# Kernel tuning notes

Measured on AMD Instinct MI355X. Metric: run time of the kernel, lower is better.

The kernel has to match this reference:

```python
import jax, jax.numpy as jnp
import numpy as np

K = 24          # num_eigh
D_MODEL = 768   # d_in == d_out
STATE = 100     # LDS state_dim
BSZ = 1
SEQ = 2048


def setup_inputs() -> dict:
    key = jax.random.key(0)
    ks = jax.random.split(key, 8)
    x = jax.random.normal(ks[0], (BSZ, SEQ, D_MODEL), dtype=jnp.float32)
    input_pos = jnp.arange(SEQ, dtype=jnp.int32)
    M_inputs = jax.random.normal(ks[1], (D_MODEL, D_MODEL), dtype=jnp.float32) * 0.02
    M_filters = jax.random.normal(ks[2], (K, D_MODEL), dtype=jnp.float32) * 0.02
    # LDS params: diagonal A (stable, |a|<1), B maps scalar input -> state,
    # C maps state -> 2K outputs, Dv is scalar-input feedthrough to 2K outputs.
    A = jax.random.uniform(ks[3], (STATE,), dtype=jnp.float32, minval=0.0, maxval=0.99)
    Bm = jax.random.normal(ks[4], (STATE,), dtype=jnp.float32) * 0.1
    C = jax.random.normal(ks[5], (STATE, 2 * K), dtype=jnp.float32) * 0.1
    Dv = jax.random.normal(ks[6], (2 * K,), dtype=jnp.float32) * 0.1
    return {"x": x, "input_pos": input_pos, "M_inputs": M_inputs,
            "M_filters": M_filters, "A": A, "Bm": Bm, "C": C, "Dv": Dv}


def reference(x, input_pos, M_inputs, M_filters, A, Bm, C, Dv):
    bsz, seq_len, d_in = x.shape
    k = M_filters.shape[0]
    # input projection (use_approx branch)
    xp = x @ M_inputs                                   # (b, s, d)
    # flatten per-channel scalar sequences: (b*d, s)
    u = xp.transpose(0, 2, 1).reshape(bsz * d_in, seq_len)
    ut = u.T                                            # (s, N) for scan over time
    h0 = jnp.zeros((bsz * d_in, A.shape[0]), dtype=xp.dtype)

    def step(h, u_t):
        # h: (N, state), u_t: (N,) scalar input per lane
        h = h * A[None, :] + u_t[:, None] * Bm[None, :]
        y = h @ C + u_t[:, None] * Dv[None, :]          # (N, 2K)
        return h, y

    _, ys = jax.lax.scan(step, h0, ut)                  # (s, N, 2K)
    # U: (b, s, 2K, d)
    U = ys.transpose(1, 0, 2).reshape(bsz, d_in, seq_len, 2 * k).transpose(0, 2, 3, 1)
    spectral_plus = jnp.einsum('bskd,kd->bsd', U[:, :, k:, :], M_filters)
    spectral_minus = jnp.einsum('bskd,kd->bsd', U[:, :, :k, :], M_filters)
    return spectral_plus + spectral_minus
```

## Files before the change

kernel.cpp:

```cpp
#include <hip/hip_runtime.h>

#define SEQ   2048
#define DM    768
#define ST    100
#define KF    24
#define NC    32
#define KJ    128
#define NJ    112
#define GK2   1536

using short8  = __attribute__((ext_vector_type(8))) short;
using float4v = __attribute__((ext_vector_type(4))) float;

__device__ __forceinline__ unsigned short bf16_rn(float x) {
    unsigned int u = __float_as_uint(x);
    unsigned int r = u + 0x7FFFu + ((u >> 16) & 1u);
    return (unsigned short)(r >> 16);
}
__device__ __forceinline__ float bf2f(unsigned short h) {
    return __uint_as_float(((unsigned int)h) << 16);
}
__device__ __forceinline__ void async16(const void* g, void* l) {
    __builtin_amdgcn_global_load_lds(
        (const __attribute__((address_space(1))) unsigned int*)g,
        (__attribute__((address_space(3))) unsigned int*)l, 16, 0, 0);
}

__global__ __launch_bounds__(256) void prep(const float* __restrict__ x,
                                            const float* __restrict__ Mi,
                                            const float* __restrict__ C,
                                            const float* __restrict__ Dv,
                                            const float* __restrict__ Mf,
                                            const float* __restrict__ Av,
                                            const float* __restrict__ Bv,
                                            unsigned short* __restrict__ Mbig,
                                            unsigned short* __restrict__ Xbig,
                                            float* __restrict__ WpT,
                                            float* __restrict__ evec,
                                            float* __restrict__ Apow,
                                            unsigned short* __restrict__ Ehi,
                                            unsigned short* __restrict__ Elo,
                                            unsigned short* __restrict__ Qhi,
                                            unsigned short* __restrict__ Qlo) {
    __shared__ float tl[64][65];
    int bid = blockIdx.x, t = threadIdx.x;
    if (bid < 144) {
        int i0 = (bid / 12) * 64, d0 = (bid % 12) * 64;
        int tx = t & 63, ty = t >> 6;
#pragma unroll
        for (int r = ty; r < 64; r += 4)
            tl[r][tx] = Mi[(i0 + r) * DM + d0 + tx];
        __syncthreads();
#pragma unroll
        for (int r = ty; r < 64; r += 4) {
            float v = tl[tx][r];
            unsigned short h = bf16_rn(v);
            unsigned short lo = bf16_rn(v - bf2f(h));
            unsigned short* row = Mbig + (size_t)(d0 + r) * GK2 + i0 + tx;
            row[0] = h; row[DM] = lo;
        }
    } else if (bid < 912) {
        int idx8 = (bid - 144) * 256 + t;
        int s = idx8 / (DM / 8), i0 = (idx8 % (DM / 8)) * 8;
        const float* xp = x + (size_t)s * DM + i0;
        float4 v0 = *(const float4*)xp;
        float4 v1 = *(const float4*)(xp + 4);
        float av[8] = {v0.x, v0.y, v0.z, v0.w, v1.x, v1.y, v1.z, v1.w};
        short8 hh;
#pragma unroll
        for (int q = 0; q < 8; ++q) hh[q] = (short)bf16_rn(av[q]);
        *(short8*)(Xbig + (size_t)s * DM + i0) = hh;
    } else if (bid < 1212) {
        int tid = (bid - 912) * 256 + t;
        if (tid < ST * DM) {
            int d = tid / ST, j = tid % ST;
            float s = 0.f;
#pragma unroll
            for (int k = 0; k < KF; ++k)
                s += (C[j * 2 * KF + k] + C[j * 2 * KF + KF + k]) * Mf[k * DM + d];
            WpT[tid] = s;
        }
        if (tid < DM) {
            float s = 0.f;
#pragma unroll
            for (int k = 0; k < KF; ++k)
                s += (Dv[k] + Dv[KF + k]) * Mf[k * DM + tid];
            evec[tid] = s;
        }
    } else {
        if (t < KJ) {
            bool ja = (t < ST);
            float a = ja ? Av[t] : 0.f;
            float b = ja ? Bv[t] : 0.f;
            float p = 1.f;
            for (int dlt = 0; dlt < 64; ++dlt) {
                if (ja) Apow[dlt * ST + t] = p;
                if (t < NJ) {
                    float v = b * p;
                    unsigned short h = bf16_rn(v);
                    Qhi[t * 64 + 63 - dlt] = h;
                    Qlo[t * 64 + 63 - dlt] = bf16_rn(v - bf2f(h));
                }
                p *= a;
                unsigned short h = bf16_rn(p);
                Ehi[dlt * KJ + t] = h;
                Elo[dlt * KJ + t] = bf16_rn(p - bf2f(h));
            }
            if (ja) Apow[64 * ST + t] = p;
        }
    }
}

__global__ __launch_bounds__(256) void gemm_mfma(const unsigned short* __restrict__ Mbig,
                                                 const unsigned short* __restrict__ Xbig,
                                                 float* __restrict__ ut0,
                                                 float* __restrict__ ut1) {
    __shared__ unsigned short As[64 * 32];
    __shared__ unsigned short Bs[64 * 32];
    int t = threadIdx.x;
    int tile = blockIdx.x;
    int d0 = (tile % (DM / 64)) * 64;
    int s0 = (tile / (DM / 64)) * 64;
    int ks = blockIdx.y;
    int kb0 = ks * DM;
    float* utp = ks ? ut1 : ut0;
    int wave = t >> 6, lane = t & 63;
    int m16 = lane & 15, quad = lane >> 4;
    int r0 = t >> 2, q0 = ((t & 3) - (t >> 3)) & 3;
    float4v acc[4];
#pragma unroll
    for (int nt = 0; nt < 4; ++nt) acc[nt] = (float4v){0.f, 0.f, 0.f, 0.f};
    for (int k0 = 0; k0 < DM; k0 += 32) {
        __syncthreads();
        async16(&Mbig[(size_t)(d0 + r0) * GK2 + kb0 + k0 + q0 * 8], &As[(size_t)t * 8]);
        async16(&Xbig[(size_t)(s0 + r0) * DM + k0 + q0 * 8], &Bs[(size_t)t * 8]);
        __syncthreads();
        int arow = wave * 16 + m16;
        int aqp = (quad + (arow >> 1)) & 3;
        short8 af = *(short8*)&As[arow * 32 + aqp * 8];
        short8 bf[4];
#pragma unroll
        for (int nt = 0; nt < 4; ++nt) {
            int brow = nt * 16 + m16;
            int bqp = (quad + (brow >> 1)) & 3;
            bf[nt] = *(short8*)&Bs[brow * 32 + bqp * 8];
        }
#pragma unroll
        for (int nt = 0; nt < 4; ++nt)
            acc[nt] = __builtin_amdgcn_mfma_f32_16x16x32_bf16(af, bf[nt], acc[nt], 0, 0, 0);
    }
#pragma unroll
    for (int nt = 0; nt < 4; ++nt) {
        int dd = d0 + wave * 16 + quad * 4;
        int ss = s0 + nt * 16 + m16;
#pragma unroll
        for (int i = 0; i < 4; ++i)
            utp[(size_t)(dd + i) * SEQ + ss] = acc[nt][i];
    }
}

__global__ __launch_bounds__(256) void scanf_k(const float* __restrict__ ut0,
                                               float* uy,
                                               const unsigned short* __restrict__ Qhi,
                                               const unsigned short* __restrict__ Qlo,
                                               const float* __restrict__ WpT,
                                               const float* __restrict__ Apow,
                                               const float* __restrict__ Bv,
                                               const float* __restrict__ evec,
                                               unsigned short* __restrict__ Ghi,
                                               unsigned short* __restrict__ Glo) {
    __shared__ float hl[64][120];
    __shared__ float kk[128];
    int t = threadIdx.x;
    int m0 = blockIdx.x * 64;
    int d0 = blockIdx.x * 2;
    if (t < 128) {
        int dlt = t & 63, dloc = t >> 6;
        const float* wrow = WpT + (d0 + dloc) * ST;
        float s = 0.f;
        for (int j = 0; j < ST; ++j)
            s = fmaf(Bv[j] * Apow[dlt * ST + j], wrow[j], s);
        kk[t] = s;
    }
    int wave = t >> 6, lane = t & 63;
    int m16 = lane & 15, quad = lane >> 4;
    {
        float4v acc[7];
#pragma unroll
        for (int nt = 0; nt < 7; ++nt) acc[nt] = (float4v){0.f, 0.f, 0.f, 0.f};
#pragma unroll
        for (int ks = 0; ks < 2; ++ks) {
            size_t ao = (size_t)(m0 + wave * 16 + m16) * 64 + ks * 32 + quad * 8;
            float4 a0 = *(const float4*)(ut0 + ao);
            float4 a1 = *(const float4*)(ut0 + ao + 4);
            float4 b0 = *(const float4*)(uy + ao);
            float4 b1 = *(const float4*)(uy + ao + 4);
            float av[8] = {a0.x + b0.x, a0.y + b0.y, a0.z + b0.z, a0.w + b0.w,
                           a1.x + b1.x, a1.y + b1.y, a1.z + b1.z, a1.w + b1.w};
            short8 ah, al;
#pragma unroll
            for (int q = 0; q < 8; ++q) {
                unsigned short h = bf16_rn(av[q]);
                ah[q] = (short)h;
                al[q] = (short)bf16_rn(av[q] - bf2f(h));
            }
#pragma unroll
            for (int nt = 0; nt < 7; ++nt) {
                int qoff = (nt * 16 + m16) * 64 + ks * 32 + quad * 8;
                short8 bh = *(const short8*)(Qhi + qoff);
                short8 bl = *(const short8*)(Qlo + qoff);
                acc[nt] = __builtin_amdgcn_mfma_f32_16x16x32_bf16(ah, bh, acc[nt], 0, 0, 0);
                acc[nt] = __builtin_amdgcn_mfma_f32_16x16x32_bf16(ah, bl, acc[nt], 0, 0, 0);
                acc[nt] = __builtin_amdgcn_mfma_f32_16x16x32_bf16(al, bh, acc[nt], 0, 0, 0);
            }
        }
#pragma unroll
        for (int nt = 0; nt < 7; ++nt)
#pragma unroll
            for (int i = 0; i < 4; ++i)
                hl[wave * 16 + quad * 4 + i][nt * 16 + m16] = acc[nt][i];
    }
    __syncthreads();
    {
        int j = t & 127, dloc = t >> 7;
        int d = d0 + dloc;
        bool ja = (j < ST);
        float a64 = ja ? Apow[64 * ST + j] : 0.f;
        float w   = ja ? WpT[d * ST + j] : 0.f;
        float hs = 0.f;
        for (int c = 0; c < NC; ++c) {
            float g = ja ? (w * hs) : 0.f;
            unsigned short gh = bf16_rn(g);
            unsigned short gl = bf16_rn(g - bf2f(gh));
            size_t go = ((size_t)c * DM + d) * KJ + j;
            Ghi[go] = gh;
            Glo[go] = gl;
            float add = ja ? hl[dloc * 32 + c][j] : 0.f;
            hs = fmaf(a64, hs, add);
        }
    }
    if (t < 64) {
        int dloc = t >> 5, c = t & 31;
        int d = d0 + dloc;
        size_t off = (size_t)d * SEQ + c * 64;
        float uu[64];
#pragma unroll
        for (int q = 0; q < 16; ++q) {
            float4 v0 = *(const float4*)(ut0 + off + q * 4);
            float4 v1 = *(const float4*)(uy + off + q * 4);
            uu[q * 4 + 0] = v0.x + v1.x; uu[q * 4 + 1] = v0.y + v1.y;
            uu[q * 4 + 2] = v0.z + v1.z; uu[q * 4 + 3] = v0.w + v1.w;
        }
        float e = evec[d];
        float y[64];
#pragma unroll
        for (int tt = 0; tt < 64; ++tt) y[tt] = e * uu[tt];
        const float* kt = &kk[dloc * 64];
#pragma unroll
        for (int dlt = 0; dlt < 64; ++dlt) {
            float k = kt[dlt];
#pragma unroll
            for (int tt = dlt; tt < 64; ++tt)
                y[tt] = fmaf(k, uu[tt - dlt], y[tt]);
        }
#pragma unroll
        for (int q = 0; q < 16; ++q) {
            float4 v = make_float4(y[q * 4 + 0], y[q * 4 + 1], y[q * 4 + 2], y[q * 4 + 3]);
            *(float4*)(uy + off + q * 4) = v;
        }
    }
}

__global__ __launch_bounds__(256) void inter(const unsigned short* __restrict__ Ehi,
                                             const unsigned short* __restrict__ Elo,
                                             const unsigned short* __restrict__ Ghi,
                                             const unsigned short* __restrict__ Glo,
                                             const float* __restrict__ yintra,
                                             float* __restrict__ out) {
    __shared__ float yl[64][68];
    int c = blockIdx.x;
    int d0 = blockIdx.y * 64;
    int t = threadIdx.x;
#pragma unroll
    for (int it = 0; it < 4; ++it) {
        int idx = t + it * 256;
        int row = idx >> 4, col4 = (idx & 15) * 4;
        float4 v = *(const float4*)&yintra[(size_t)(d0 + row) * SEQ + c * 64 + col4];
        yl[col4 + 0][row] = v.x;
        yl[col4 + 1][row] = v.y;
        yl[col4 + 2][row] = v.z;
        yl[col4 + 3][row] = v.w;
    }
    __syncthreads();
    int wave = t >> 6, lane = t & 63;
    int wn = wave * 16;
    int m16 = lane & 15, quad = lane >> 4;
    float4v acc[4];
#pragma unroll
    for (int mt = 0; mt < 4; ++mt) acc[mt] = (float4v){0.f, 0.f, 0.f, 0.f};
#pragma unroll
    for (int ks = 0; ks < 4; ++ks) {
        size_t gb = ((size_t)c * DM + d0 + wn + m16) * KJ + ks * 32 + quad * 8;
        short8 bh = *(const short8*)(Ghi + gb);
        short8 bl = *(const short8*)(Glo + gb);
#pragma unroll
        for (int mt = 0; mt < 4; ++mt) {
            int eo = (mt * 16 + m16) * KJ + ks * 32 + quad * 8;
            short8 ah = *(const short8*)(Ehi + eo);
            short8 al = *(const short8*)(Elo + eo);
            acc[mt] = __builtin_amdgcn_mfma_f32_16x16x32_bf16(ah, bh, acc[mt], 0, 0, 0);
            acc[mt] = __builtin_amdgcn_mfma_f32_16x16x32_bf16(ah, bl, acc[mt], 0, 0, 0);
            acc[mt] = __builtin_amdgcn_mfma_f32_16x16x32_bf16(al, bh, acc[mt], 0, 0, 0);
        }
    }
#pragma unroll
    for (int mt = 0; mt < 4; ++mt) {
        int tt = mt * 16 + quad * 4;
        int dcol = wn + m16;
#pragma unroll
        for (int i = 0; i < 4; ++i) {
            float v = acc[mt][i] + yl[tt + i][dcol];
            out[(size_t)(c * 64 + tt + i) * DM + d0 + dcol] = v;
        }
    }
}

extern "C" void kernel_launch(void* const* d_in, const int* in_sizes, int n_in,
                              void* d_out, int out_size, void* d_ws, size_t ws_size,
                              hipStream_t stream) {
    const float* x  = (const float*)d_in[0];
    const float* Mi = (const float*)d_in[2];
    const float* Mf = (const float*)d_in[3];
    const float* Av = (const float*)d_in[4];
    const float* Bv = (const float*)d_in[5];
    const float* C  = (const float*)d_in[6];
    const float* Dv = (const float*)d_in[7];
    float* out = (float*)d_out;

    float* ut0    = (float*)d_ws;
    float* WpT    = ut0 + (size_t)DM * SEQ;
    float* ev     = WpT + DM * ST;
    float* Apow   = ev + DM;
    float* ut1    = Apow + 65 * ST;
    unsigned short* Mbig = (unsigned short*)(ut1 + (size_t)DM * SEQ);
    unsigned short* Xbig = Mbig + (size_t)DM * GK2;
    unsigned short* Ehi  = Xbig + (size_t)SEQ * DM;
    unsigned short* Elo  = Ehi + 64 * KJ;
    unsigned short* Qhi  = Elo + 64 * KJ;
    unsigned short* Qlo  = Qhi + NJ * 64;
    unsigned short* Ghi  = Qlo + NJ * 64;
    unsigned short* Glo  = Ghi + (size_t)NC * DM * KJ;

    prep<<<1213, 256, 0, stream>>>(x, Mi, C, Dv, Mf, Av, Bv, Mbig, Xbig,
                                   WpT, ev, Apow, Ehi, Elo, Qhi, Qlo);
    gemm_mfma<<<dim3((DM / 64) * (SEQ / 64), 2), 256, 0, stream>>>(Mbig, Xbig, ut0, ut1);
    scanf_k<<<384, 256, 0, stream>>>(ut0, ut1, Qhi, Qlo, WpT, Apow, Bv, ev, Ghi, Glo);
    inter<<<dim3(NC, DM / 64), 256, 0, stream>>>(Ehi, Elo, Ghi, Glo, ut1, out);
}
```

Baseline: 137.4 us.

## Replace split-bf16 hi/lo MFMA with single-pass fp16 MFMA throughout

Replaces the split bf16 (hi+lo) representation with single fp16 values across all stages. The input projection now runs as one K=768 GEMM with 64-wide K tiles instead of two split-K passes whose outputs had to be summed. The scan and inter-chunk MFMAs drop from three products to one, and the lo-part buffers disappear. This cuts MFMA work, memory traffic and one workspace buffer, at the cost of fp16 precision and range, which may increase numerical error against the fp32 reference.

```diff
diff --git a/kernel.cpp b/kernel.cpp
--- a/kernel.cpp
+++ b/kernel.cpp
@@ -7,18 +7,15 @@
 #define NC    32
 #define KJ    128
 #define NJ    112
-#define GK2   1536
-
-using short8  = __attribute__((ext_vector_type(8))) short;
+
+using half8   = __attribute__((ext_vector_type(8))) _Float16;
 using float4v = __attribute__((ext_vector_type(4))) float;
-
-__device__ __forceinline__ unsigned short bf16_rn(float x) {
-    unsigned int u = __float_as_uint(x);
-    unsigned int r = u + 0x7FFFu + ((u >> 16) & 1u);
-    return (unsigned short)(r >> 16);
-}
-__device__ __forceinline__ float bf2f(unsigned short h) {
-    return __uint_as_float(((unsigned int)h) << 16);
+using ush8    = __attribute__((ext_vector_type(8))) short;
+
+__device__ __forceinline__ unsigned short f2h(float v) {
+    union { _Float16 h; unsigned short u; } cv;
+    cv.h = (_Float16)v;
+    return cv.u;
 }
 __device__ __forceinline__ void async16(const void* g, void* l) {
     __builtin_amdgcn_global_load_lds(
@@ -33,15 +30,13 @@
                                             const float* __restrict__ Mf,
                                             const float* __restrict__ Av,
                                             const float* __restrict__ Bv,
-                                            unsigned short* __restrict__ Mbig,
-                                            unsigned short* __restrict__ Xbig,
+                                            unsigned short* __restrict__ Mh,
+                                            unsigned short* __restrict__ Xh,
                                             float* __restrict__ WpT,
                                             float* __restrict__ evec,
                                             float* __restrict__ Apow,
-                                            unsigned short* __restrict__ Ehi,
-                                            unsigned short* __restrict__ Elo,
-                                            unsigned short* __restrict__ Qhi,
-                                            unsigned short* __restrict__ Qlo) {
+                                            unsigned short* __restrict__ Eh,
+                                            unsigned short* __restrict__ Qh) {
     __shared__ float tl[64][65];
     int bid = blockIdx.x, t = threadIdx.x;
     if (bid < 144) {
@@ -52,13 +47,8 @@
             tl[r][tx] = Mi[(i0 + r) * DM + d0 + tx];
         __syncthreads();
 #pragma unroll
-        for (int r = ty; r < 64; r += 4) {
-            float v = tl[tx][r];
-            unsigned short h = bf16_rn(v);
-            unsigned short lo = bf16_rn(v - bf2f(h));
-            unsigned short* row = Mbig + (size_t)(d0 + r) * GK2 + i0 + tx;
-            row[0] = h; row[DM] = lo;
-        }
+        for (int r = ty; r < 64; r += 4)
+            Mh[(size_t)(d0 + r) * DM + i0 + tx] = f2h(tl[tx][r]);
     } else if (bid < 912) {
         int idx8 = (bid - 144) * 256 + t;
         int s = idx8 / (DM / 8), i0 = (idx8 % (DM / 8)) * 8;
@@ -66,10 +56,10 @@
         float4 v0 = *(const float4*)xp;
         float4 v1 = *(const float4*)(xp + 4);
         float av[8] = {v0.x, v0.y, v0.z, v0.w, v1.x, v1.y, v1.z, v1.w};
-        short8 hh;
-#pragma unroll
-        for (int q = 0; q < 8; ++q) hh[q] = (short)bf16_rn(av[q]);
-        *(short8*)(Xbig + (size_t)s * DM + i0) = hh;
+        ush8 hh;
+#pragma unroll
+        for (int q = 0; q < 8; ++q) hh[q] = (short)f2h(av[q]);
+        *(ush8*)(Xh + (size_t)s * DM + i0) = hh;
     } else if (bid < 1212) {
         int tid = (bid - 912) * 256 + t;
         if (tid < ST * DM) {
@@ -95,59 +85,55 @@
             float p = 1.f;
             for (int dlt = 0; dlt < 64; ++dlt) {
                 if (ja) Apow[dlt * ST + t] = p;
-                if (t < NJ) {
-                    float v = b * p;
-                    unsigned short h = bf16_rn(v);
-                    Qhi[t * 64 + 63 - dlt] = h;
-                    Qlo[t * 64 + 63 - dlt] = bf16_rn(v - bf2f(h));
-                }
+                if (t < NJ) Qh[t * 64 + 63 - dlt] = f2h(b * p);
                 p *= a;
-                unsigned short h = bf16_rn(p);
-                Ehi[dlt * KJ + t] = h;
-                Elo[dlt * KJ + t] = bf16_rn(p - bf2f(h));
+                Eh[dlt * KJ + t] = f2h(p);
             }
             if (ja) Apow[64 * ST + t] = p;
         }
     }
 }
 
-__global__ __launch_bounds__(256) void gemm_mfma(const unsigned short* __restrict__ Mbig,
-                                                 const unsigned short* __restrict__ Xbig,
-                                                 float* __restrict__ ut0,
-                                                 float* __restrict__ ut1) {
-    __shared__ unsigned short As[64 * 32];
-    __shared__ unsigned short Bs[64 * 32];
+__global__ __launch_bounds__(256) void gemm_mfma(const unsigned short* __restrict__ Mh,
+                                                 const unsigned short* __restrict__ Xh,
+                                                 float* __restrict__ ut) {
+    __shared__ unsigned short As[64 * 64];
+    __shared__ unsigned short Bs[64 * 64];
     int t = threadIdx.x;
     int tile = blockIdx.x;
     int d0 = (tile % (DM / 64)) * 64;
     int s0 = (tile / (DM / 64)) * 64;
-    int ks = blockIdx.y;
-    int kb0 = ks * DM;
-    float* utp = ks ? ut1 : ut0;
     int wave = t >> 6, lane = t & 63;
     int m16 = lane & 15, quad = lane >> 4;
-    int r0 = t >> 2, q0 = ((t & 3) - (t >> 3)) & 3;
+    int r0 = t >> 3,         q0 = ((t & 7) - r0) & 7;
+    int r1 = (t + 256) >> 3, q1 = (((t + 256) & 7) - r1) & 7;
     float4v acc[4];
 #pragma unroll
     for (int nt = 0; nt < 4; ++nt) acc[nt] = (float4v){0.f, 0.f, 0.f, 0.f};
-    for (int k0 = 0; k0 < DM; k0 += 32) {
+    for (int k0 = 0; k0 < DM; k0 += 64) {
         __syncthreads();
-        async16(&Mbig[(size_t)(d0 + r0) * GK2 + kb0 + k0 + q0 * 8], &As[(size_t)t * 8]);
-        async16(&Xbig[(size_t)(s0 + r0) * DM + k0 + q0 * 8], &Bs[(size_t)t * 8]);
+        async16(&Mh[(size_t)(d0 + r0) * DM + k0 + q0 * 8], &As[(size_t)t * 8]);
+        async16(&Xh[(size_t)(s0 + r0) * DM + k0 + q0 * 8], &Bs[(size_t)t * 8]);
+        async16(&Mh[(size_t)(d0 + r1) * DM + k0 + q1 * 8], &As[(size_t)(t + 256) * 8]);
+        async16(&Xh[(size_t)(s0 + r1) * DM + k0 + q1 * 8], &Bs[(size_t)(t + 256) * 8]);
         __syncthreads();
         int arow = wave * 16 + m16;
-        int aqp = (quad + (arow >> 1)) & 3;
-        short8 af = *(short8*)&As[arow * 32 + aqp * 8];
-        short8 bf[4];
+        half8 af[2], bf[4][2];
+#pragma unroll
+        for (int h = 0; h < 2; ++h)
+            af[h] = *(half8*)&As[arow * 64 + (((h * 4 + quad) + arow) & 7) * 8];
 #pragma unroll
         for (int nt = 0; nt < 4; ++nt) {
             int brow = nt * 16 + m16;
-            int bqp = (quad + (brow >> 1)) & 3;
-            bf[nt] = *(short8*)&Bs[brow * 32 + bqp * 8];
-        }
-#pragma unroll
-        for (int nt = 0; nt < 4; ++nt)
-            acc[nt] = __builtin_amdgcn_mfma_f32_16x16x32_bf16(af, bf[nt], acc[nt], 0, 0, 0);
+#pragma unroll
+            for (int h = 0; h < 2; ++h)
+                bf[nt][h] = *(half8*)&Bs[brow * 64 + (((h * 4 + quad) + brow) & 7) * 8];
+        }
+#pragma unroll
+        for (int h = 0; h < 2; ++h)
+#pragma unroll
+            for (int nt = 0; nt < 4; ++nt)
+                acc[nt] = __builtin_amdgcn_mfma_f32_16x16x32_f16(af[h], bf[nt][h], acc[nt], 0, 0, 0);
     }
 #pragma unroll
     for (int nt = 0; nt < 4; ++nt) {
@@ -155,20 +141,17 @@
         int ss = s0 + nt * 16 + m16;
 #pragma unroll
         for (int i = 0; i < 4; ++i)
-            utp[(size_t)(dd + i) * SEQ + ss] = acc[nt][i];
-    }
-}
-
-__global__ __launch_bounds__(256) void scanf_k(const float* __restrict__ ut0,
-                                               float* uy,
-                                               const unsigned short* __restrict__ Qhi,
-                                               const unsigned short* __restrict__ Qlo,
+            ut[(size_t)(dd + i) * SEQ + ss] = acc[nt][i];
+    }
+}
+
+__global__ __launch_bounds__(256) void scanf_k(float* ut,
+                                               const unsigned short* __restrict__ Qh,
                                                const float* __restrict__ WpT,
                                                const float* __restrict__ Apow,
                                                const float* __restrict__ Bv,
                                                const float* __restrict__ evec,
-                                               unsigned short* __restrict__ Ghi,
-                                               unsigned short* __restrict__ Glo) {
+                                               unsigned short* __restrict__ Gh) {
     __shared__ float hl[64][120];
     __shared__ float kk[128];
     int t = threadIdx.x;
@@ -191,27 +174,16 @@
 #pragma unroll
         for (int ks = 0; ks < 2; ++ks) {
             size_t ao = (size_t)(m0 + wave * 16 + m16) * 64 + ks * 32 + quad * 8;
-            float4 a0 = *(const float4*)(ut0 + ao);
-            float4 a1 = *(const float4*)(ut0 + ao + 4);
-            float4 b0 = *(const float4*)(uy + ao);
-            float4 b1 = *(const float4*)(uy + ao + 4);
-            float av[8] = {a0.x + b0.x, a0.y + b0.y, a0.z + b0.z, a0.w + b0.w,
-                           a1.x + b1.x, a1.y + b1.y, a1.z + b1.z, a1.w + b1.w};
-            short8 ah, al;
-#pragma unroll
-            for (int q = 0; q < 8; ++q) {
-                unsigned short h = bf16_rn(av[q]);
-                ah[q] = (short)h;
-                al[q] = (short)bf16_rn(av[q] - bf2f(h));
-            }
+            float4 a0 = *(const float4*)(ut + ao);
+            float4 a1 = *(const float4*)(ut + ao + 4);
+            float av[8] = {a0.x, a0.y, a0.z, a0.w, a1.x, a1.y, a1.z, a1.w};
+            half8 ah;
+#pragma unroll
+            for (int q = 0; q < 8; ++q) ah[q] = (_Float16)av[q];
 #pragma unroll
             for (int nt = 0; nt < 7; ++nt) {
-                int qoff = (nt * 16 + m16) * 64 + ks * 32 + quad * 8;
-                short8 bh = *(const short8*)(Qhi + qoff);
-                short8 bl = *(const short8*)(Qlo + qoff);
-                acc[nt] = __builtin_amdgcn_mfma_f32_16x16x32_bf16(ah, bh, acc[nt], 0, 0, 0);
-                acc[nt] = __builtin_amdgcn_mfma_f32_16x16x32_bf16(ah, bl, acc[nt], 0, 0, 0);
-                acc[nt] = __builtin_amdgcn_mfma_f32_16x16x32_bf16(al, bh, acc[nt], 0, 0, 0);
+                half8 bh = *(const half8*)(Qh + (nt * 16 + m16) * 64 + ks * 32 + quad * 8);
+                acc[nt] = __builtin_amdgcn_mfma_f32_16x16x32_f16(ah, bh, acc[nt], 0, 0, 0);
             }
         }
 #pragma unroll
@@ -229,12 +201,7 @@
         float w   = ja ? WpT[d * ST + j] : 0.f;
         float hs = 0.f;
         for (int c = 0; c < NC; ++c) {
-            float g = ja ? (w * hs) : 0.f;
-            unsigned short gh = bf16_rn(g);
-            unsigned short gl = bf16_rn(g - bf2f(gh));
-            size_t go = ((size_t)c * DM + d) * KJ + j;
-            Ghi[go] = gh;
-            Glo[go] = gl;
+            Gh[((size_t)c * DM + d) * KJ + j] = f2h(w * hs);
             float add = ja ? hl[dloc * 32 + c][j] : 0.f;
             hs = fmaf(a64, hs, add);
         }
@@ -246,10 +213,9 @@
         float uu[64];
 #pragma unroll
         for (int q = 0; q < 16; ++q) {
-            float4 v0 = *(const float4*)(ut0 + off + q * 4);
-            float4 v1 = *(const float4*)(uy + off + q * 4);
-            uu[q * 4 + 0] = v0.x + v1.x; uu[q * 4 + 1] = v0.y + v1.y;
-            uu[q * 4 + 2] = v0.z + v1.z; uu[q * 4 + 3] = v0.w + v1.w;
+            float4 v = *(const float4*)(ut + off + q * 4);
+            uu[q * 4 + 0] = v.x; uu[q * 4 + 1] = v.y;
+            uu[q * 4 + 2] = v.z; uu[q * 4 + 3] = v.w;
         }
         float e = evec[d];
         float y[64];
@@ -266,15 +232,13 @@
 #pragma unroll
         for (int q = 0; q < 16; ++q) {
             float4 v = make_float4(y[q * 4 + 0], y[q * 4 + 1], y[q * 4 + 2], y[q * 4 + 3]);
-            *(float4*)(uy + off + q * 4) = v;
-        }
-    }
-}
-
-__global__ __launch_bounds__(256) void inter(const unsigned short* __restrict__ Ehi,
-                                             const unsigned short* __restrict__ Elo,
-                                             const unsigned short* __restrict__ Ghi,
-                                             const unsigned short* __restrict__ Glo,
+            *(float4*)(ut + off + q * 4) = v;
+        }
+    }
+}
+
+__global__ __launch_bounds__(256) void inter(const unsigned short* __restrict__ Eh,
+                                             const unsigned short* __restrict__ Gh,
                                              const float* __restrict__ yintra,
                                              float* __restrict__ out) {
     __shared__ float yl[64][68];
@@ -300,17 +264,11 @@
     for (int mt = 0; mt < 4; ++mt) acc[mt] = (float4v){0.f, 0.f, 0.f, 0.f};
 #pragma unroll
     for (int ks = 0; ks < 4; ++ks) {
-        size_t gb = ((size_t)c * DM + d0 + wn + m16) * KJ + ks * 32 + quad * 8;
-        short8 bh = *(const short8*)(Ghi + gb);
-        short8 bl = *(const short8*)(Glo + gb);
+        half8 bh = *(const half8*)(Gh + ((size_t)c * DM + d0 + wn + m16) * KJ + ks * 32 + quad * 8);
 #pragma unroll
         for (int mt = 0; mt < 4; ++mt) {
-            int eo = (mt * 16 + m16) * KJ + ks * 32 + quad * 8;
-            short8 ah = *(const short8*)(Ehi + eo);
-            short8 al = *(const short8*)(Elo + eo);
-            acc[mt] = __builtin_amdgcn_mfma_f32_16x16x32_bf16(ah, bh, acc[mt], 0, 0, 0);
-            acc[mt] = __builtin_amdgcn_mfma_f32_16x16x32_bf16(ah, bl, acc[mt], 0, 0, 0);
-            acc[mt] = __builtin_amdgcn_mfma_f32_16x16x32_bf16(al, bh, acc[mt], 0, 0, 0);
+            half8 ah = *(const half8*)(Eh + (mt * 16 + m16) * KJ + ks * 32 + quad * 8);
+            acc[mt] = __builtin_amdgcn_mfma_f32_16x16x32_f16(ah, bh, acc[mt], 0, 0, 0);
         }
     }
 #pragma unroll
@@ -337,23 +295,19 @@
     const float* Dv = (const float*)d_in[7];
     float* out = (float*)d_out;
 
-    float* ut0    = (float*)d_ws;
-    float* WpT    = ut0 + (size_t)DM * SEQ;
-    float* ev     = WpT + DM * ST;
-    float* Apow   = ev + DM;
-    float* ut1    = Apow + 65 * ST;
-    unsigned short* Mbig = (unsigned short*)(ut1 + (size_t)DM * SEQ);
-    unsigned short* Xbig = Mbig + (size_t)DM * GK2;
-    unsigned short* Ehi  = Xbig + (size_t)SEQ * DM;
-    unsigned short* Elo  = Ehi + 64 * KJ;
-    unsigned short* Qhi  = Elo + 64 * KJ;
-    unsigned short* Qlo  = Qhi + NJ * 64;
-    unsigned short* Ghi  = Qlo + NJ * 64;
-    unsigned short* Glo  = Ghi + (size_t)NC * DM * KJ;
-
-    prep<<<1213, 256, 0, stream>>>(x, Mi, C, Dv, Mf, Av, Bv, Mbig, Xbig,
-                                   WpT, ev, Apow, Ehi, Elo, Qhi, Qlo);
-    gemm_mfma<<<dim3((DM / 64) * (SEQ / 64), 2), 256, 0, stream>>>(Mbig, Xbig, ut0, ut1);
-    scanf_k<<<384, 256, 0, stream>>>(ut0, ut1, Qhi, Qlo, WpT, Apow, Bv, ev, Ghi, Glo);
-    inter<<<dim3(NC, DM / 64), 256, 0, stream>>>(Ehi, Elo, Ghi, Glo, ut1, out);
-}
+    float* ut   = (float*)d_ws;
+    float* WpT  = ut + (size_t)DM * SEQ;
+    float* ev   = WpT + DM * ST;
+    float* Apow = ev + DM;
+    unsigned short* Mh = (unsigned short*)(Apow + 65 * ST);
+    unsigned short* Xh = Mh + (size_t)DM * DM;
+    unsigned short* Eh = Xh + (size_t)SEQ * DM;
+    unsigned short* Qh = Eh + 64 * KJ;
+    unsigned short* Gh = Qh + NJ * 64;
+
+    prep<<<1213, 256, 0, stream>>>(x, Mi, C, Dv, Mf, Av, Bv, Mh, Xh,
+                                   WpT, ev, Apow, Eh, Qh);
+    gemm_mfma<<<(DM / 64) * (SEQ / 64), 256, 0, stream>>>(Mh, Xh, ut);
+    scanf_k<<<384, 256, 0, stream>>>(ut, Qh, WpT, Apow, Bv, ev, Gh);
+    inter<<<dim3(NC, DM / 64), 256, 0, stream>>>(Eh, Gh, ut, out);
+}
```

Measured after the change: 114.2 us, median of 2. -16.9%, faster.
